# Kernel tuning notes

Hardware: AMD Instinct MI355X
Metric: run time of the kernel (lower is better)

The kernel has to match this reference:

```python
import jax, jax.numpy as jnp
import numpy as np

DIM, DK, DV = 1024, 128, 128
B, S = 4, 2048

def setup_inputs() -> dict:
    key = jax.random.key(0)
    ks = jax.random.split(key, 7)
    s = lambda d: 1.0 / np.sqrt(d)
    return {
        "x":  jax.random.normal(ks[0], (B, S, DIM), dtype=jnp.float32),
        "Wq": jax.random.normal(ks[1], (DIM, DK), dtype=jnp.float32) * s(DIM),
        "bq": jax.random.normal(ks[2], (DK,), dtype=jnp.float32) * 0.02,
        "Wk": jax.random.normal(ks[3], (DIM, DK), dtype=jnp.float32) * s(DIM),
        "bk": jax.random.normal(ks[4], (DK,), dtype=jnp.float32) * 0.02,
        "Wv": jax.random.normal(ks[5], (DIM, DV), dtype=jnp.float32) * s(DIM),
        "bv": jax.random.normal(ks[6], (DV,), dtype=jnp.float32) * 0.02,
    }

def reference(x, Wq, bq, Wk, bk, Wv, bv):
    scale = DK ** (-0.5)
    q = x @ Wq + bq                      # [B,S,DK]
    k = x @ Wk + bk                      # [B,S,DK]
    v = x @ Wv + bv                      # [B,S,DV]
    attn = jnp.einsum('bsd,btd->bst', q, k) * scale  # [B,S,S]
    attn = jax.nn.softmax(attn, axis=-1)
    return jnp.einsum('bst,btd->bsd', attn, v)       # [B,S,DV]
```

## Files before the change

kernel.cpp:

```cpp
#include <hip/hip_runtime.h>

typedef unsigned short u16;
typedef unsigned int u32;
typedef __bf16 bf16;
typedef __bf16 bf16x8 __attribute__((ext_vector_type(8)));
typedef float f32x4 __attribute__((ext_vector_type(4)));
typedef u32 u32x4 __attribute__((ext_vector_type(4)));


__device__ __forceinline__ void gl_lds16(const void* g, void* l) {
  __builtin_amdgcn_global_load_lds(
      (const __attribute__((address_space(1))) void*)g,
      (__attribute__((address_space(3))) void*)l, 16, 0, 0);
}
__device__ __forceinline__ u16 bfbits(float f) {
  return __builtin_bit_cast(u16, (bf16)f);
}
__device__ __forceinline__ u32 pk2(float lo, float hi) {
  return (u32)bfbits(lo) | ((u32)bfbits(hi) << 16);
}
__device__ __forceinline__ float fexp2(float x) {
  return __builtin_amdgcn_exp2f(x);
}

__global__ __launch_bounds__(256) void wprep_kernel(
    const float* __restrict__ Wq, const float* __restrict__ Wk,
    const float* __restrict__ Wv, u16* __restrict__ Wt) {
  __shared__ u16 st[64][72];
  const int tid = threadIdx.x;
  const int m = blockIdx.x >> 5, rem = blockIdx.x & 31, kt = rem >> 1, nt = rem & 1;
  const float* W = (m == 0) ? Wq : (m == 1) ? Wk : Wv;
  const int k0 = kt * 64, n0 = nt * 64;
#pragma unroll
  for (int i = 0; i < 4; ++i) {
    int kk = i * 16 + (tid >> 4), nn = (tid & 15) * 4;
    f32x4 w = *(const f32x4*)&W[(size_t)(k0 + kk) * 128 + n0 + nn];
    st[kk][nn]     = bfbits(w[0]); st[kk][nn + 1] = bfbits(w[1]);
    st[kk][nn + 2] = bfbits(w[2]); st[kk][nn + 3] = bfbits(w[3]);
  }
  __syncthreads();
#pragma unroll
  for (int i = 0; i < 4; ++i) {
    int nn = i * 16 + (tid >> 4), kk = (tid & 15) * 4;
    ushort4 u;
    u.x = st[kk][nn]; u.y = st[kk + 1][nn]; u.z = st[kk + 2][nn]; u.w = st[kk + 3][nn];
    *(ushort4*)&Wt[(size_t)m * 131072 + (size_t)(n0 + nn) * 1024 + k0 + kk] = u;
  }
}

__global__ __launch_bounds__(256) void qkv_gemm(
    const float* __restrict__ x, const u16* __restrict__ Wt,
    const float* __restrict__ bq, const float* __restrict__ bk, const float* __restrict__ bv,
    u16* __restrict__ qb, u16* __restrict__ kb, u16* __restrict__ vt)
{
  __shared__ __attribute__((aligned(16))) u16 sxb[2][64 * 64];
  __shared__ __attribute__((aligned(16))) u16 sw[2][128 * 64];
  const int tid = threadIdx.x, wid = tid >> 6, lane = tid & 63;
  const int g = lane >> 4, q16 = lane & 15;
  const int m = blockIdx.y;
  const int row0 = blockIdx.x * 64;
  const u16* W = Wt + (size_t)m * 131072;
  const int wr = wid >> 1, wc = wid & 1;

  const float* xsrc[2]; int xdo[2];
#pragma unroll
  for (int i = 0; i < 2; ++i) {
    int fc = i * 256 + tid, r = fc >> 3, c = fc & 7;
    xsrc[i] = x + (size_t)(row0 + r) * 1024 + c * 8;
    xdo[i] = r * 64 + ((c ^ (r & 7)) << 3);
  }

  f32x4 xst[2][2];
  auto XLOAD = [&](int k0) {
#pragma unroll
    for (int i = 0; i < 2; ++i) {
      xst[i][0] = *(const f32x4*)(xsrc[i] + k0);
      xst[i][1] = *(const f32x4*)(xsrc[i] + k0 + 4);
    }
  };
  auto XWRITE = [&](int buf) {
#pragma unroll
    for (int i = 0; i < 2; ++i) {
      u32x4 v = {pk2(xst[i][0][0], xst[i][0][1]), pk2(xst[i][0][2], xst[i][0][3]),
                 pk2(xst[i][1][0], xst[i][1][1]), pk2(xst[i][1][2], xst[i][1][3])};
      *(u32x4*)&sxb[buf][xdo[i]] = v;
    }
  };
  auto WSTAGE = [&](int buf, int k0) {
#pragma unroll
    for (int i = 0; i < 4; ++i) {
      int fc = i * 256 + tid; int r = fc >> 3, c = fc & 7;
      gl_lds16(W + (size_t)r * 1024 + k0 + ((c ^ (r & 7)) << 3),
               (char*)&sw[buf][0] + fc * 16);
    }
  };

  f32x4 acc[2][4] = {};
  XLOAD(0); WSTAGE(0, 0);
  asm volatile("s_waitcnt vmcnt(0)" ::: "memory");
  XWRITE(0);
  __syncthreads();
  int cur = 0;

  for (int kt = 0; kt < 16; ++kt) {
    if (kt < 15) { XLOAD((kt + 1) * 64); WSTAGE(cur ^ 1, (kt + 1) * 64); }
    const u16* sxc = &sxb[cur][0];
    const u16* swc = &sw[cur][0];
#pragma unroll
    for (int ks = 0; ks < 2; ++ks) {
      bf16x8 af[2], bfr[4];
#pragma unroll
      for (int mr = 0; mr < 2; ++mr) {
        int row = wr * 32 + mr * 16 + q16;
        int ch = (ks * 4 + g) ^ (row & 7);
        af[mr] = *(const bf16x8*)(sxc + row * 64 + ch * 8);
      }
#pragma unroll
      for (int nr = 0; nr < 4; ++nr) {
        int row = wc * 64 + nr * 16 + q16;
        int ch = (ks * 4 + g) ^ (row & 7);
        bfr[nr] = *(const bf16x8*)(swc + row * 64 + ch * 8);
      }
#pragma unroll
      for (int mr = 0; mr < 2; ++mr)
#pragma unroll
        for (int nr = 0; nr < 4; ++nr)
          acc[mr][nr] = __builtin_amdgcn_mfma_f32_16x16x32_bf16(af[mr], bfr[nr], acc[mr][nr], 0, 0, 0);
    }
    if (kt < 15) {
      asm volatile("s_waitcnt vmcnt(0)" ::: "memory");
      XWRITE(cur ^ 1);
      __syncthreads();
      cur ^= 1;
    }
  }

  const float* bias = (m == 0) ? bq : (m == 1) ? bk : bv;
  u16* qk = (m == 0) ? qb : kb;
#pragma unroll
  for (int mr = 0; mr < 2; ++mr) {
#pragma unroll
    for (int nr = 0; nr < 4; ++nr) {
      int col = wc * 64 + nr * 16 + q16;
      float bc = bias[col];
      int grow = row0 + wr * 32 + mr * 16 + g * 4;
      if (m == 2) {
        int bb = grow >> 11;
        int sbase = ((grow & 2047) & ~31) | (g * 8 + mr * 4);
        ushort4 u;
        u.x = bfbits(acc[mr][nr][0] + bc);
        u.y = bfbits(acc[mr][nr][1] + bc);
        u.z = bfbits(acc[mr][nr][2] + bc);
        u.w = bfbits(acc[mr][nr][3] + bc);
        *(ushort4*)&vt[(size_t)bb * 262144 + (size_t)col * 2048 + sbase] = u;
      } else {
#pragma unroll
        for (int r = 0; r < 4; ++r)
          qk[(size_t)(grow + r) * 128 + col] = bfbits(acc[mr][nr][r] + bc);
      }
    }
  }
}

union ALDS {
  u16 stg[8][8192];
  struct {
    float oc[8][32 * 132];
    float l[8][32];
    float linv[32];
  } cb;
};

__global__ __launch_bounds__(512) void attn_kernel(
    const u16* __restrict__ qb, const u16* __restrict__ kb, const u16* __restrict__ vt,
    float* __restrict__ out)
{
  __shared__ __attribute__((aligned(16))) ALDS lds;
  const int tid = threadIdx.x, wid = tid >> 6, lane = tid & 63;
  const int g = lane >> 4, q16 = lane & 15;
  const int qt = blockIdx.x, b = blockIdx.y;
  const size_t qgA = (size_t)b * 2048 + qt * 32;
  const u16* kbw = kb + ((size_t)b * 2048 + wid * 256) * 128;
  const u16* vbw = vt + (size_t)b * 262144 + wid * 256;
  u16* skw = &lds.stg[wid][0];
  u16* svw = &lds.stg[wid][4096];
  const float scale2 = 0.08838834764831845f * 1.4426950408889634f;

  bf16x8 qfA[4], qfB[4];
#pragma unroll
  for (int kg = 0; kg < 4; ++kg) {
    qfA[kg] = *(const bf16x8*)&qb[(qgA + q16) * 128 + kg * 32 + g * 8];
    qfB[kg] = *(const bf16x8*)&qb[(qgA + 16 + q16) * 128 + kg * 32 + g * 8];
  }

  auto SK = [&](int t) {
#pragma unroll
    for (int i = 0; i < 8; ++i) {
      int fc = i * 64 + lane; int r = fc >> 4, c = fc & 15;
      gl_lds16(kbw + (size_t)(t * 32 + r) * 128 + ((c ^ (r & 7)) << 3),
               (char*)skw + fc * 16);
    }
  };
  auto SV = [&](int t) {
#pragma unroll
    for (int i = 0; i < 8; ++i) {
      int fc = i * 64 + lane; int r = fc >> 2, c = fc & 3;
      int h = (r ^ (r >> 2)) & 3;
      gl_lds16(vbw + (size_t)r * 2048 + t * 32 + ((c ^ h) << 3),
               (char*)svw + fc * 16);
    }
  };

  float lA = 0.f, lB = 0.f;
  f32x4 accA[8] = {}, accB[8] = {};

  SK(0); SV(0);
  for (int t = 0; t < 8; ++t) {
    asm volatile("s_waitcnt vmcnt(8)" ::: "memory");

    f32x4 sTa[2] = {}, sTb[2] = {};
#pragma unroll
    for (int kg = 0; kg < 4; ++kg)
#pragma unroll
      for (int jg = 0; jg < 2; ++jg) {
        int row = jg * 16 + q16;
        int ch = (kg * 4 + g) ^ (row & 7);
        bf16x8 kf = *(const bf16x8*)(skw + row * 128 + ch * 8);
        sTa[jg] = __builtin_amdgcn_mfma_f32_16x16x32_bf16(kf, qfA[kg], sTa[jg], 0, 0, 0);
        sTb[jg] = __builtin_amdgcn_mfma_f32_16x16x32_bf16(kf, qfB[kg], sTb[jg], 0, 0, 0);
      }
    __builtin_amdgcn_sched_barrier(0);
    if (t < 7) SK(t + 1);

    u32 WpA[2][2], WpB[2][2];
#pragma unroll
    for (int jg = 0; jg < 2; ++jg) {
      float e0 = fexp2(sTa[jg][0] * scale2);
      float e1 = fexp2(sTa[jg][1] * scale2);
      float e2 = fexp2(sTa[jg][2] * scale2);
      float e3 = fexp2(sTa[jg][3] * scale2);
      lA += (e0 + e1) + (e2 + e3);
      WpA[jg][0] = pk2(e0, e1);
      WpA[jg][1] = pk2(e2, e3);
    }
#pragma unroll
    for (int jg = 0; jg < 2; ++jg) {
      float e0 = fexp2(sTb[jg][0] * scale2);
      float e1 = fexp2(sTb[jg][1] * scale2);
      float e2 = fexp2(sTb[jg][2] * scale2);
      float e3 = fexp2(sTb[jg][3] * scale2);
      lB += (e0 + e1) + (e2 + e3);
      WpB[jg][0] = pk2(e0, e1);
      WpB[jg][1] = pk2(e2, e3);
    }

    u32x4 wa = {WpA[0][0], WpA[0][1], WpA[1][0], WpA[1][1]};
    u32x4 wb = {WpB[0][0], WpB[0][1], WpB[1][0], WpB[1][1]};
    bf16x8 pA = __builtin_bit_cast(bf16x8, wa);
    bf16x8 pB = __builtin_bit_cast(bf16x8, wb);

    if (t < 7) { asm volatile("s_waitcnt vmcnt(8)" ::: "memory"); }
    else       { asm volatile("s_waitcnt vmcnt(0)" ::: "memory"); }

#pragma unroll
    for (int dg = 0; dg < 8; ++dg) {
      int row = dg * 16 + q16;
      int ch = g ^ ((row ^ (row >> 2)) & 3);
      bf16x8 vf = *(const bf16x8*)(svw + row * 32 + ch * 8);
      accA[dg] = __builtin_amdgcn_mfma_f32_16x16x32_bf16(vf, pA, accA[dg], 0, 0, 0);
      accB[dg] = __builtin_amdgcn_mfma_f32_16x16x32_bf16(vf, pB, accB[dg], 0, 0, 0);
    }
    __builtin_amdgcn_sched_barrier(0);
    if (t < 7) SV(t + 1);
  }

  lA += __shfl_xor(lA, 16); lA += __shfl_xor(lA, 32);
  lB += __shfl_xor(lB, 16); lB += __shfl_xor(lB, 32);

  __syncthreads();
  {
    float* ocp = &lds.cb.oc[wid][0];
#pragma unroll
    for (int dg = 0; dg < 8; ++dg) {
      *(f32x4*)&ocp[q16 * 132 + dg * 16 + g * 4] = accA[dg];
      *(f32x4*)&ocp[(16 + q16) * 132 + dg * 16 + g * 4] = accB[dg];
    }
    if (g == 0) {
      lds.cb.l[wid][q16] = lA;
      lds.cb.l[wid][16 + q16] = lB;
    }
  }
  __syncthreads();
  if (tid < 32) {
    int q = tid;
    float s = 0.f;
#pragma unroll
    for (int w = 0; w < 8; ++w) s += lds.cb.l[w][q];
    lds.cb.linv[q] = 1.0f / s;
  }
  __syncthreads();
#pragma unroll
  for (int h = 0; h < 2; ++h) {
    int idx = h * 512 + tid;
    int q = idx >> 5, d4 = idx & 31;
    f32x4 v = {0.f, 0.f, 0.f, 0.f};
#pragma unroll
    for (int w = 0; w < 8; ++w)
      v += *(const f32x4*)&lds.cb.oc[w][q * 132 + d4 * 4];
    v *= lds.cb.linv[q];
    *(f32x4*)&out[((size_t)b * 2048 + qt * 32 + q) * 128 + d4 * 4] = v;
  }
}

extern "C" void kernel_launch(void* const* d_in, const int* in_sizes, int n_in,
                              void* d_out, int out_size, void* d_ws, size_t ws_size,
                              hipStream_t stream)
{
  (void)in_sizes; (void)n_in; (void)out_size; (void)ws_size;
  const float* x  = (const float*)d_in[0];
  const float* Wq = (const float*)d_in[1];
  const float* bq = (const float*)d_in[2];
  const float* Wk = (const float*)d_in[3];
  const float* bk = (const float*)d_in[4];
  const float* Wv = (const float*)d_in[5];
  const float* bv = (const float*)d_in[6];
  char* ws = (char*)d_ws;
  u16* qbuf  = (u16*)(ws);
  u16* kbuf  = (u16*)(ws + (2u << 20));
  u16* vtbuf = (u16*)(ws + (4u << 20));
  u16* Wt    = (u16*)(ws + (6u << 20));

  wprep_kernel<<<96, 256, 0, stream>>>(Wq, Wk, Wv, Wt);
  qkv_gemm<<<dim3(128, 3), 256, 0, stream>>>(x, Wt, bq, bk, bv, qbuf, kbuf, vtbuf);
  attn_kernel<<<dim3(64, 4), 512, 0, stream>>>(qbuf, kbuf, vtbuf, (float*)d_out);
}
```

Measured before the change: 54.86 us.

## Fuse weight prep, QKV GEMM and attention into one persistent kernel with grid barriers

```diff
diff --git a/kernel.cpp b/kernel.cpp
--- a/kernel.cpp
+++ b/kernel.cpp
@@ -23,292 +23,313 @@
   return __builtin_amdgcn_exp2f(x);
 }
 
-__global__ __launch_bounds__(256) void wprep_kernel(
-    const float* __restrict__ Wq, const float* __restrict__ Wk,
-    const float* __restrict__ Wv, u16* __restrict__ Wt) {
-  __shared__ u16 st[64][72];
-  const int tid = threadIdx.x;
-  const int m = blockIdx.x >> 5, rem = blockIdx.x & 31, kt = rem >> 1, nt = rem & 1;
-  const float* W = (m == 0) ? Wq : (m == 1) ? Wk : Wv;
-  const int k0 = kt * 64, n0 = nt * 64;
-#pragma unroll
-  for (int i = 0; i < 4; ++i) {
-    int kk = i * 16 + (tid >> 4), nn = (tid & 15) * 4;
-    f32x4 w = *(const f32x4*)&W[(size_t)(k0 + kk) * 128 + n0 + nn];
-    st[kk][nn]     = bfbits(w[0]); st[kk][nn + 1] = bfbits(w[1]);
-    st[kk][nn + 2] = bfbits(w[2]); st[kk][nn + 3] = bfbits(w[3]);
+union FLDS {
+  struct { u16 st[2][64 * 72]; } wp;
+  struct { u16 sxb[2][2][64 * 64]; u16 sw[2][2][128 * 64]; } qk;
+  struct { u16 stg[8][8192]; } at;
+  struct { float oc[8][32 * 132]; float l[8][32]; float linv[32]; } cb;
+};
+
+__device__ __forceinline__ void gridbar(u32* bar, u32 nblk) {
+  __syncthreads();
+  if (threadIdx.x == 0) {
+    __threadfence();
+    u32 old = __hip_atomic_fetch_add(&bar[0], 1u, __ATOMIC_ACQ_REL,
+                                     __HIP_MEMORY_SCOPE_AGENT);
+    if (old == nblk - 1) {
+      __hip_atomic_store(&bar[1], 1u, __ATOMIC_RELEASE, __HIP_MEMORY_SCOPE_AGENT);
+    } else {
+      while (__hip_atomic_load(&bar[1], __ATOMIC_ACQUIRE,
+                               __HIP_MEMORY_SCOPE_AGENT) == 0u)
+        __builtin_amdgcn_s_sleep(2);
+    }
   }
   __syncthreads();
-#pragma unroll
-  for (int i = 0; i < 4; ++i) {
-    int nn = i * 16 + (tid >> 4), kk = (tid & 15) * 4;
-    ushort4 u;
-    u.x = st[kk][nn]; u.y = st[kk + 1][nn]; u.z = st[kk + 2][nn]; u.w = st[kk + 3][nn];
-    *(ushort4*)&Wt[(size_t)m * 131072 + (size_t)(n0 + nn) * 1024 + k0 + kk] = u;
+}
+
+__global__ __launch_bounds__(512) void fused_kernel(
+    const float* __restrict__ x,
+    const float* __restrict__ Wq, const float* __restrict__ bq,
+    const float* __restrict__ Wk, const float* __restrict__ bk,
+    const float* __restrict__ Wv, const float* __restrict__ bv,
+    u16* __restrict__ qb, u16* __restrict__ kb, u16* __restrict__ vt,
+    u16* __restrict__ Wt, u32* __restrict__ bars, float* __restrict__ out)
+{
+  __shared__ __attribute__((aligned(16))) FLDS lds;
+  const int tid = threadIdx.x;
+
+  if (blockIdx.x < 48) {
+    const int e = tid >> 8, etid = tid & 255;
+    const int tile = blockIdx.x * 2 + e;
+    const int m = tile >> 5, rem = tile & 31, kt = rem >> 1, nt = rem & 1;
+    const float* W = (m == 0) ? Wq : (m == 1) ? Wk : Wv;
+    const int k0 = kt * 64, n0 = nt * 64;
+    u16* st = &lds.wp.st[e][0];
+#pragma unroll
+    for (int i = 0; i < 4; ++i) {
+      int kk = i * 16 + (etid >> 4), nn = (etid & 15) * 4;
+      f32x4 w = *(const f32x4*)&W[(size_t)(k0 + kk) * 128 + n0 + nn];
+      st[kk * 72 + nn]     = bfbits(w[0]); st[kk * 72 + nn + 1] = bfbits(w[1]);
+      st[kk * 72 + nn + 2] = bfbits(w[2]); st[kk * 72 + nn + 3] = bfbits(w[3]);
+    }
+    __syncthreads();
+#pragma unroll
+    for (int i = 0; i < 4; ++i) {
+      int nn = i * 16 + (etid >> 4), kk = (etid & 15) * 4;
+      ushort4 u;
+      u.x = st[kk * 72 + nn]; u.y = st[(kk + 1) * 72 + nn];
+      u.z = st[(kk + 2) * 72 + nn]; u.w = st[(kk + 3) * 72 + nn];
+      *(ushort4*)&Wt[(size_t)m * 131072 + (size_t)(n0 + nn) * 1024 + k0 + kk] = u;
+    }
   }
-}
-
-__global__ __launch_bounds__(256) void qkv_gemm(
-    const float* __restrict__ x, const u16* __restrict__ Wt,
-    const float* __restrict__ bq, const float* __restrict__ bk, const float* __restrict__ bv,
-    u16* __restrict__ qb, u16* __restrict__ kb, u16* __restrict__ vt)
-{
-  __shared__ __attribute__((aligned(16))) u16 sxb[2][64 * 64];
-  __shared__ __attribute__((aligned(16))) u16 sw[2][128 * 64];
-  const int tid = threadIdx.x, wid = tid >> 6, lane = tid & 63;
-  const int g = lane >> 4, q16 = lane & 15;
-  const int m = blockIdx.y;
-  const int row0 = blockIdx.x * 64;
-  const u16* W = Wt + (size_t)m * 131072;
-  const int wr = wid >> 1, wc = wid & 1;
-
-  const float* xsrc[2]; int xdo[2];
-#pragma unroll
-  for (int i = 0; i < 2; ++i) {
-    int fc = i * 256 + tid, r = fc >> 3, c = fc & 7;
-    xsrc[i] = x + (size_t)(row0 + r) * 1024 + c * 8;
-    xdo[i] = r * 64 + ((c ^ (r & 7)) << 3);
+  gridbar(bars, 256);
+
+  if (blockIdx.x < 192) {
+    const int e = tid >> 8, etid = tid & 255;
+    const int wid = etid >> 6, lane = etid & 63;
+    const int g = lane >> 4, q16 = lane & 15;
+    const int vtile = blockIdx.x * 2 + e;
+    const int m = vtile >> 7;
+    const int row0 = (vtile & 127) * 64;
+    const u16* W = Wt + (size_t)m * 131072;
+    const int wr = wid >> 1, wc = wid & 1;
+
+    const float* xsrc[2]; int xdo[2];
+#pragma unroll
+    for (int i = 0; i < 2; ++i) {
+      int fc = i * 256 + etid, r = fc >> 3, c = fc & 7;
+      xsrc[i] = x + (size_t)(row0 + r) * 1024 + c * 8;
+      xdo[i] = r * 64 + ((c ^ (r & 7)) << 3);
+    }
+
+    f32x4 xst[2][2];
+    auto XLOAD = [&](int k0) {
+#pragma unroll
+      for (int i = 0; i < 2; ++i) {
+        xst[i][0] = *(const f32x4*)(xsrc[i] + k0);
+        xst[i][1] = *(const f32x4*)(xsrc[i] + k0 + 4);
+      }
+    };
+    auto XWRITE = [&](int buf) {
+#pragma unroll
+      for (int i = 0; i < 2; ++i) {
+        u32x4 v = {pk2(xst[i][0][0], xst[i][0][1]), pk2(xst[i][0][2], xst[i][0][3]),
+                   pk2(xst[i][1][0], xst[i][1][1]), pk2(xst[i][1][2], xst[i][1][3])};
+        *(u32x4*)&lds.qk.sxb[e][buf][xdo[i]] = v;
+      }
+    };
+    auto WSTAGE = [&](int buf, int k0) {
+#pragma unroll
+      for (int i = 0; i < 4; ++i) {
+        int fc = i * 256 + etid; int r = fc >> 3, c = fc & 7;
+        gl_lds16(W + (size_t)r * 1024 + k0 + ((c ^ (r & 7)) << 3),
+                 (char*)&lds.qk.sw[e][buf][0] + fc * 16);
+      }
+    };
+
+    f32x4 acc[2][4] = {};
+    XLOAD(0); WSTAGE(0, 0);
+    asm volatile("s_waitcnt vmcnt(0)" ::: "memory");
+    XWRITE(0);
+    __syncthreads();
+    int cur = 0;
+
+    for (int kt = 0; kt < 16; ++kt) {
+      if (kt < 15) { XLOAD((kt + 1) * 64); WSTAGE(cur ^ 1, (kt + 1) * 64); }
+      const u16* sxc = &lds.qk.sxb[e][cur][0];
+      const u16* swc = &lds.qk.sw[e][cur][0];
+#pragma unroll
+      for (int ks = 0; ks < 2; ++ks) {
+        bf16x8 af[2], bfr[4];
+#pragma unroll
+        for (int mr = 0; mr < 2; ++mr) {
+          int row = wr * 32 + mr * 16 + q16;
+          int ch = (ks * 4 + g) ^ (row & 7);
+          af[mr] = *(const bf16x8*)(sxc + row * 64 + ch * 8);
+        }
+#pragma unroll
+        for (int nr = 0; nr < 4; ++nr) {
+          int row = wc * 64 + nr * 16 + q16;
+          int ch = (ks * 4 + g) ^ (row & 7);
+          bfr[nr] = *(const bf16x8*)(swc + row * 64 + ch * 8);
+        }
+#pragma unroll
+        for (int mr = 0; mr < 2; ++mr)
+#pragma unroll
+          for (int nr = 0; nr < 4; ++nr)
+            acc[mr][nr] = __builtin_amdgcn_mfma_f32_16x16x32_bf16(af[mr], bfr[nr], acc[mr][nr], 0, 0, 0);
+      }
+      if (kt < 15) {
+        asm volatile("s_waitcnt vmcnt(0)" ::: "memory");
+        XWRITE(cur ^ 1);
+        __syncthreads();
+        cur ^= 1;
+      }
+    }
+
+    const float* bias = (m == 0) ? bq : (m == 1) ? bk : bv;
+    u16* qk = (m == 0) ? qb : kb;
+#pragma unroll
+    for (int mr = 0; mr < 2; ++mr) {
+#pragma unroll
+      for (int nr = 0; nr < 4; ++nr) {
+        int col = wc * 64 + nr * 16 + q16;
+        float bc = bias[col];
+        int grow = row0 + wr * 32 + mr * 16 + g * 4;
+        if (m == 2) {
+          int bb = grow >> 11;
+          int sbase = ((grow & 2047) & ~31) | (g * 8 + mr * 4);
+          ushort4 u;
+          u.x = bfbits(acc[mr][nr][0] + bc);
+          u.y = bfbits(acc[mr][nr][1] + bc);
+          u.z = bfbits(acc[mr][nr][2] + bc);
+          u.w = bfbits(acc[mr][nr][3] + bc);
+          *(ushort4*)&vt[(size_t)bb * 262144 + (size_t)col * 2048 + sbase] = u;
+        } else {
+#pragma unroll
+          for (int r = 0; r < 4; ++r)
+            qk[(size_t)(grow + r) * 128 + col] = bfbits(acc[mr][nr][r] + bc);
+        }
+      }
+    }
   }
-
-  f32x4 xst[2][2];
-  auto XLOAD = [&](int k0) {
-#pragma unroll
-    for (int i = 0; i < 2; ++i) {
-      xst[i][0] = *(const f32x4*)(xsrc[i] + k0);
-      xst[i][1] = *(const f32x4*)(xsrc[i] + k0 + 4);
-    }
-  };
-  auto XWRITE = [&](int buf) {
-#pragma unroll
-    for (int i = 0; i < 2; ++i) {
-      u32x4 v = {pk2(xst[i][0][0], xst[i][0][1]), pk2(xst[i][0][2], xst[i][0][3]),
-                 pk2(xst[i][1][0], xst[i][1][1]), pk2(xst[i][1][2], xst[i][1][3])};
-      *(u32x4*)&sxb[buf][xdo[i]] = v;
-    }
-  };
-  auto WSTAGE = [&](int buf, int k0) {
-#pragma unroll
-    for (int i = 0; i < 4; ++i) {
-      int fc = i * 256 + tid; int r = fc >> 3, c = fc & 7;
-      gl_lds16(W + (size_t)r * 1024 + k0 + ((c ^ (r & 7)) << 3),
-               (char*)&sw[buf][0] + fc * 16);
-    }
-  };
-
-  f32x4 acc[2][4] = {};
-  XLOAD(0); WSTAGE(0, 0);
-  asm volatile("s_waitcnt vmcnt(0)" ::: "memory");
-  XWRITE(0);
-  __syncthreads();
-  int cur = 0;
-
-  for (int kt = 0; kt < 16; ++kt) {
-    if (kt < 15) { XLOAD((kt + 1) * 64); WSTAGE(cur ^ 1, (kt + 1) * 64); }
-    const u16* sxc = &sxb[cur][0];
-    const u16* swc = &sw[cur][0];
-#pragma unroll
-    for (int ks = 0; ks < 2; ++ks) {
-      bf16x8 af[2], bfr[4];
-#pragma unroll
-      for (int mr = 0; mr < 2; ++mr) {
-        int row = wr * 32 + mr * 16 + q16;
-        int ch = (ks * 4 + g) ^ (row & 7);
-        af[mr] = *(const bf16x8*)(sxc + row * 64 + ch * 8);
-      }
-#pragma unroll
-      for (int nr = 0; nr < 4; ++nr) {
-        int row = wc * 64 + nr * 16 + q16;
-        int ch = (ks * 4 + g) ^ (row & 7);
-        bfr[nr] = *(const bf16x8*)(swc + row * 64 + ch * 8);
-      }
-#pragma unroll
-      for (int mr = 0; mr < 2; ++mr)
-#pragma unroll
-        for (int nr = 0; nr < 4; ++nr)
-          acc[mr][nr] = __builtin_amdgcn_mfma_f32_16x16x32_bf16(af[mr], bfr[nr], acc[mr][nr], 0, 0, 0);
-    }
-    if (kt < 15) {
-      asm volatile("s_waitcnt vmcnt(0)" ::: "memory");
-      XWRITE(cur ^ 1);
-      __syncthreads();
-      cur ^= 1;
-    }
-  }
-
-  const float* bias = (m == 0) ? bq : (m == 1) ? bk : bv;
-  u16* qk = (m == 0) ? qb : kb;
-#pragma unroll
-  for (int mr = 0; mr < 2; ++mr) {
-#pragma unroll
-    for (int nr = 0; nr < 4; ++nr) {
-      int col = wc * 64 + nr * 16 + q16;
-      float bc = bias[col];
-      int grow = row0 + wr * 32 + mr * 16 + g * 4;
-      if (m == 2) {
-        int bb = grow >> 11;
-        int sbase = ((grow & 2047) & ~31) | (g * 8 + mr * 4);
-        ushort4 u;
-        u.x = bfbits(acc[mr][nr][0] + bc);
-        u.y = bfbits(acc[mr][nr][1] + bc);
-        u.z = bfbits(acc[mr][nr][2] + bc);
-        u.w = bfbits(acc[mr][nr][3] + bc);
-        *(ushort4*)&vt[(size_t)bb * 262144 + (size_t)col * 2048 + sbase] = u;
-      } else {
-#pragma unroll
-        for (int r = 0; r < 4; ++r)
-          qk[(size_t)(grow + r) * 128 + col] = bfbits(acc[mr][nr][r] + bc);
-      }
-    }
-  }
-}
-
-union ALDS {
-  u16 stg[8][8192];
-  struct {
-    float oc[8][32 * 132];
-    float l[8][32];
-    float linv[32];
-  } cb;
-};
-
-__global__ __launch_bounds__(512) void attn_kernel(
-    const u16* __restrict__ qb, const u16* __restrict__ kb, const u16* __restrict__ vt,
-    float* __restrict__ out)
-{
-  __shared__ __attribute__((aligned(16))) ALDS lds;
-  const int tid = threadIdx.x, wid = tid >> 6, lane = tid & 63;
-  const int g = lane >> 4, q16 = lane & 15;
-  const int qt = blockIdx.x, b = blockIdx.y;
-  const size_t qgA = (size_t)b * 2048 + qt * 32;
-  const u16* kbw = kb + ((size_t)b * 2048 + wid * 256) * 128;
-  const u16* vbw = vt + (size_t)b * 262144 + wid * 256;
-  u16* skw = &lds.stg[wid][0];
-  u16* svw = &lds.stg[wid][4096];
-  const float scale2 = 0.08838834764831845f * 1.4426950408889634f;
-
-  bf16x8 qfA[4], qfB[4];
-#pragma unroll
-  for (int kg = 0; kg < 4; ++kg) {
-    qfA[kg] = *(const bf16x8*)&qb[(qgA + q16) * 128 + kg * 32 + g * 8];
-    qfB[kg] = *(const bf16x8*)&qb[(qgA + 16 + q16) * 128 + kg * 32 + g * 8];
-  }
-
-  auto SK = [&](int t) {
-#pragma unroll
-    for (int i = 0; i < 8; ++i) {
-      int fc = i * 64 + lane; int r = fc >> 4, c = fc & 15;
-      gl_lds16(kbw + (size_t)(t * 32 + r) * 128 + ((c ^ (r & 7)) << 3),
-               (char*)skw + fc * 16);
-    }
-  };
-  auto SV = [&](int t) {
-#pragma unroll
-    for (int i = 0; i < 8; ++i) {
-      int fc = i * 64 + lane; int r = fc >> 2, c = fc & 3;
-      int h = (r ^ (r >> 2)) & 3;
-      gl_lds16(vbw + (size_t)r * 2048 + t * 32 + ((c ^ h) << 3),
-               (char*)svw + fc * 16);
-    }
-  };
-
-  float lA = 0.f, lB = 0.f;
-  f32x4 accA[8] = {}, accB[8] = {};
-
-  SK(0); SV(0);
-  for (int t = 0; t < 8; ++t) {
-    asm volatile("s_waitcnt vmcnt(8)" ::: "memory");
-
-    f32x4 sTa[2] = {}, sTb[2] = {};
-#pragma unroll
-    for (int kg = 0; kg < 4; ++kg)
+  gridbar(bars + 32, 256);
+
+  {
+    const int wid = tid >> 6, lane = tid & 63;
+    const int g = lane >> 4, q16 = lane & 15;
+    const int qt = blockIdx.x & 63, b = blockIdx.x >> 6;
+    const size_t qgA = (size_t)b * 2048 + qt * 32;
+    const u16* kbw = kb + ((size_t)b * 2048 + wid * 256) * 128;
+    const u16* vbw = vt + (size_t)b * 262144 + wid * 256;
+    u16* skw = &lds.at.stg[wid][0];
+    u16* svw = &lds.at.stg[wid][4096];
+    const float scale2 = 0.08838834764831845f * 1.4426950408889634f;
+
+    bf16x8 qfA[4], qfB[4];
+#pragma unroll
+    for (int kg = 0; kg < 4; ++kg) {
+      qfA[kg] = *(const bf16x8*)&qb[(qgA + q16) * 128 + kg * 32 + g * 8];
+      qfB[kg] = *(const bf16x8*)&qb[(qgA + 16 + q16) * 128 + kg * 32 + g * 8];
+    }
+
+    auto SK = [&](int t) {
+#pragma unroll
+      for (int i = 0; i < 8; ++i) {
+        int fc = i * 64 + lane; int r = fc >> 4, c = fc & 15;
+        gl_lds16(kbw + (size_t)(t * 32 + r) * 128 + ((c ^ (r & 7)) << 3),
+                 (char*)skw + fc * 16);
+      }
+    };
+    auto SV = [&](int t) {
+#pragma unroll
+      for (int i = 0; i < 8; ++i) {
+        int fc = i * 64 + lane; int r = fc >> 2, c = fc & 3;
+        int h = (r ^ (r >> 2)) & 3;
+        gl_lds16(vbw + (size_t)r * 2048 + t * 32 + ((c ^ h) << 3),
+                 (char*)svw + fc * 16);
+      }
+    };
+
+    float lA = 0.f, lB = 0.f;
+    f32x4 accA[8] = {}, accB[8] = {};
+
+    SK(0); SV(0);
+    for (int t = 0; t < 8; ++t) {
+      asm volatile("s_waitcnt vmcnt(8)" ::: "memory");
+
+      f32x4 sTa[2] = {}, sTb[2] = {};
+#pragma unroll
+      for (int kg = 0; kg < 4; ++kg)
+#pragma unroll
+        for (int jg = 0; jg < 2; ++jg) {
+          int row = jg * 16 + q16;
+          int ch = (kg * 4 + g) ^ (row & 7);
+          bf16x8 kf = *(const bf16x8*)(skw + row * 128 + ch * 8);
+          sTa[jg] = __builtin_amdgcn_mfma_f32_16x16x32_bf16(kf, qfA[kg], sTa[jg], 0, 0, 0);
+          sTb[jg] = __builtin_amdgcn_mfma_f32_16x16x32_bf16(kf, qfB[kg], sTb[jg], 0, 0, 0);
+        }
+      __builtin_amdgcn_sched_barrier(0);
+      if (t < 7) SK(t + 1);
+
+      u32 WpA[2][2], WpB[2][2];
 #pragma unroll
       for (int jg = 0; jg < 2; ++jg) {
-        int row = jg * 16 + q16;
-        int ch = (kg * 4 + g) ^ (row & 7);
-        bf16x8 kf = *(const bf16x8*)(skw + row * 128 + ch * 8);
-        sTa[jg] = __builtin_amdgcn_mfma_f32_16x16x32_bf16(kf, qfA[kg], sTa[jg], 0, 0, 0);
-        sTb[jg] = __builtin_amdgcn_mfma_f32_16x16x32_bf16(kf, qfB[kg], sTb[jg], 0, 0, 0);
-      }
-    __builtin_amdgcn_sched_barrier(0);
-    if (t < 7) SK(t + 1);
-
-    u32 WpA[2][2], WpB[2][2];
-#pragma unroll
-    for (int jg = 0; jg < 2; ++jg) {
-      float e0 = fexp2(sTa[jg][0] * scale2);
-      float e1 = fexp2(sTa[jg][1] * scale2);
-      float e2 = fexp2(sTa[jg][2] * scale2);
-      float e3 = fexp2(sTa[jg][3] * scale2);
-      lA += (e0 + e1) + (e2 + e3);
-      WpA[jg][0] = pk2(e0, e1);
-      WpA[jg][1] = pk2(e2, e3);
-    }
-#pragma unroll
-    for (int jg = 0; jg < 2; ++jg) {
-      float e0 = fexp2(sTb[jg][0] * scale2);
-      float e1 = fexp2(sTb[jg][1] * scale2);
-      float e2 = fexp2(sTb[jg][2] * scale2);
-      float e3 = fexp2(sTb[jg][3] * scale2);
-      lB += (e0 + e1) + (e2 + e3);
-      WpB[jg][0] = pk2(e0, e1);
-      WpB[jg][1] = pk2(e2, e3);
-    }
-
-    u32x4 wa = {WpA[0][0], WpA[0][1], WpA[1][0], WpA[1][1]};
-    u32x4 wb = {WpB[0][0], WpB[0][1], WpB[1][0], WpB[1][1]};
-    bf16x8 pA = __builtin_bit_cast(bf16x8, wa);
-    bf16x8 pB = __builtin_bit_cast(bf16x8, wb);
-
-    if (t < 7) { asm volatile("s_waitcnt vmcnt(8)" ::: "memory"); }
-    else       { asm volatile("s_waitcnt vmcnt(0)" ::: "memory"); }
-
-#pragma unroll
-    for (int dg = 0; dg < 8; ++dg) {
-      int row = dg * 16 + q16;
-      int ch = g ^ ((row ^ (row >> 2)) & 3);
-      bf16x8 vf = *(const bf16x8*)(svw + row * 32 + ch * 8);
-      accA[dg] = __builtin_amdgcn_mfma_f32_16x16x32_bf16(vf, pA, accA[dg], 0, 0, 0);
-      accB[dg] = __builtin_amdgcn_mfma_f32_16x16x32_bf16(vf, pB, accB[dg], 0, 0, 0);
-    }
-    __builtin_amdgcn_sched_barrier(0);
-    if (t < 7) SV(t + 1);
-  }
-
-  lA += __shfl_xor(lA, 16); lA += __shfl_xor(lA, 32);
-  lB += __shfl_xor(lB, 16); lB += __shfl_xor(lB, 32);
-
-  __syncthreads();
-  {
-    float* ocp = &lds.cb.oc[wid][0];
-#pragma unroll
-    for (int dg = 0; dg < 8; ++dg) {
-      *(f32x4*)&ocp[q16 * 132 + dg * 16 + g * 4] = accA[dg];
-      *(f32x4*)&ocp[(16 + q16) * 132 + dg * 16 + g * 4] = accB[dg];
-    }
-    if (g == 0) {
-      lds.cb.l[wid][q16] = lA;
-      lds.cb.l[wid][16 + q16] = lB;
-    }
-  }
-  __syncthreads();
-  if (tid < 32) {
-    int q = tid;
-    float s = 0.f;
-#pragma unroll
-    for (int w = 0; w < 8; ++w) s += lds.cb.l[w][q];
-    lds.cb.linv[q] = 1.0f / s;
-  }
-  __syncthreads();
-#pragma unroll
-  for (int h = 0; h < 2; ++h) {
-    int idx = h * 512 + tid;
-    int q = idx >> 5, d4 = idx & 31;
-    f32x4 v = {0.f, 0.f, 0.f, 0.f};
-#pragma unroll
-    for (int w = 0; w < 8; ++w)
-      v += *(const f32x4*)&lds.cb.oc[w][q * 132 + d4 * 4];
-    v *= lds.cb.linv[q];
-    *(f32x4*)&out[((size_t)b * 2048 + qt * 32 + q) * 128 + d4 * 4] = v;
+        float e0 = fexp2(sTa[jg][0] * scale2);
+        float e1 = fexp2(sTa[jg][1] * scale2);
+        float e2 = fexp2(sTa[jg][2] * scale2);
+        float e3 = fexp2(sTa[jg][3] * scale2);
+        lA += (e0 + e1) + (e2 + e3);
+        WpA[jg][0] = pk2(e0, e1);
+        WpA[jg][1] = pk2(e2, e3);
+      }
+#pragma unroll
+      for (int jg = 0; jg < 2; ++jg) {
+        float e0 = fexp2(sTb[jg][0] * scale2);
+        float e1 = fexp2(sTb[jg][1] * scale2);
+        float e2 = fexp2(sTb[jg][2] * scale2);
+        float e3 = fexp2(sTb[jg][3] * scale2);
+        lB += (e0 + e1) + (e2 + e3);
+        WpB[jg][0] = pk2(e0, e1);
+        WpB[jg][1] = pk2(e2, e3);
+      }
+
+      u32x4 wa = {WpA[0][0], WpA[0][1], WpA[1][0], WpA[1][1]};
+      u32x4 wb = {WpB[0][0], WpB[0][1], WpB[1][0], WpB[1][1]};
+      bf16x8 pA = __builtin_bit_cast(bf16x8, wa);
+      bf16x8 pB = __builtin_bit_cast(bf16x8, wb);
+
+      if (t < 7) { asm volatile("s_waitcnt vmcnt(8)" ::: "memory"); }
+      else       { asm volatile("s_waitcnt vmcnt(0)" ::: "memory"); }
+
+#pragma unroll
+      for (int dg = 0; dg < 8; ++dg) {
+        int row = dg * 16 + q16;
+        int ch = g ^ ((row ^ (row >> 2)) & 3);
+        bf16x8 vf = *(const bf16x8*)(svw + row * 32 + ch * 8);
+        accA[dg] = __builtin_amdgcn_mfma_f32_16x16x32_bf16(vf, pA, accA[dg], 0, 0, 0);
+        accB[dg] = __builtin_amdgcn_mfma_f32_16x16x32_bf16(vf, pB, accB[dg], 0, 0, 0);
+      }
+      __builtin_amdgcn_sched_barrier(0);
+      if (t < 7) SV(t + 1);
+    }
+
+    lA += __shfl_xor(lA, 16); lA += __shfl_xor(lA, 32);
+    lB += __shfl_xor(lB, 16); lB += __shfl_xor(lB, 32);
+
+    __syncthreads();
+    {
+      float* ocp = &lds.cb.oc[wid][0];
+#pragma unroll
+      for (int dg = 0; dg < 8; ++dg) {
+        *(f32x4*)&ocp[q16 * 132 + dg * 16 + g * 4] = accA[dg];
+        *(f32x4*)&ocp[(16 + q16) * 132 + dg * 16 + g * 4] = accB[dg];
+      }
+      if (g == 0) {
+        lds.cb.l[wid][q16] = lA;
+        lds.cb.l[wid][16 + q16] = lB;
+      }
+    }
+    __syncthreads();
+    if (tid < 32) {
+      int q = tid;
+      float s = 0.f;
+#pragma unroll
+      for (int w = 0; w < 8; ++w) s += lds.cb.l[w][q];
+      lds.cb.linv[q] = 1.0f / s;
+    }
+    __syncthreads();
+#pragma unroll
+    for (int h = 0; h < 2; ++h) {
+      int idx = h * 512 + tid;
+      int q = idx >> 5, d4 = idx & 31;
+      f32x4 v = {0.f, 0.f, 0.f, 0.f};
+#pragma unroll
+      for (int w = 0; w < 8; ++w)
+        v += *(const f32x4*)&lds.cb.oc[w][q * 132 + d4 * 4];
+      v *= lds.cb.linv[q];
+      *(f32x4*)&out[((size_t)b * 2048 + qt * 32 + q) * 128 + d4 * 4] = v;
+    }
   }
 }
 
@@ -329,8 +350,9 @@
   u16* kbuf  = (u16*)(ws + (2u << 20));
   u16* vtbuf = (u16*)(ws + (4u << 20));
   u16* Wt    = (u16*)(ws + (6u << 20));
-
-  wprep_kernel<<<96, 256, 0, stream>>>(Wq, Wk, Wv, Wt);
-  qkv_gemm<<<dim3(128, 3), 256, 0, stream>>>(x, Wt, bq, bk, bv, qbuf, kbuf, vtbuf);
-  attn_kernel<<<dim3(64, 4), 512, 0, stream>>>(qbuf, kbuf, vtbuf, (float*)d_out);
-}
+  u32* bars  = (u32*)(ws + (7u << 20));
+
+  hipMemsetAsync((void*)bars, 0, 256, stream);
+  fused_kernel<<<256, 512, 0, stream>>>(x, Wq, bq, Wk, bk, Wv, bv,
+                                        qbuf, kbuf, vtbuf, Wt, bars, (float*)d_out);
+}
```

Result: slower. 131.5 us (+139.6%).
